# Kernel optimization log

Measured on AMD Instinct MI355X. Metric: run time of the kernel, lower is better.

Reference implementation:

```python
import jax, jax.numpy as jnp
import numpy as np

B, C_IN, C_OUT, H, W = 32, 256, 256, 56, 56
RATE = 0.5
K = int(C_OUT * (1.0 - RATE))  # 128 channels zeroed
BN_EPS = 1e-5


def setup_inputs() -> dict:
    key = jax.random.key(0)
    ks = jax.random.split(key, 4)
    return {
        "x": jax.random.normal(ks[0], (B, C_IN, H, W), dtype=jnp.float32),
        "conv_w": jax.random.normal(ks[1], (C_OUT, C_IN, 3, 3), dtype=jnp.float32) * 0.05,
        "gate_w": jax.random.normal(ks[2], (C_OUT, C_IN), dtype=jnp.float32) * 0.05,
        "gate_b": jnp.ones((C_OUT,), dtype=jnp.float32),
        "bn_gamma": jnp.ones((C_OUT,), dtype=jnp.float32),
        "bn_beta": jnp.zeros((C_OUT,), dtype=jnp.float32),
        "bn_mean": jnp.zeros((C_OUT,), dtype=jnp.float32),
        "bn_var": jnp.ones((C_OUT,), dtype=jnp.float32),
    }


def reference(x, conv_w, gate_w, gate_b, bn_gamma, bn_beta, bn_mean, bn_var):
    # conv2: 3x3, stride 1, padding 1, no bias  -> [B, C_OUT, H, W]
    y = jax.lax.conv_general_dilated(
        x, conv_w, window_strides=(1, 1), padding=((1, 1), (1, 1)),
        dimension_numbers=("NCHW", "OIHW", "NCHW"))
    # BatchNorm2d (eval mode: running stats)
    inv = bn_gamma / jnp.sqrt(bn_var + BN_EPS)
    y = y * inv[None, :, None, None] + (bn_beta - bn_mean * inv)[None, :, None, None]
    # use_relu=True
    y = jax.nn.relu(y)
    # gate: global abs-avg-pool -> linear -> relu   [B, C_OUT]
    s = jnp.mean(jnp.abs(x), axis=(2, 3))  # [B, C_IN]
    g = jax.nn.relu(s @ gate_w.T + gate_b)
    # zero the K smallest gate values per row (topk of -g), then renormalize
    _, idx = jax.lax.top_k(-g, K)  # indices of K smallest
    t = g.at[jnp.arange(B)[:, None], idx].set(0.0)
    t = t / jnp.sum(t, axis=1, keepdims=True) * C_OUT
    # broadcast channel mask
    return y * t[:, :, None, None]
```

## Files before the change

kernel.cpp:

```cpp
#include <hip/hip_runtime.h>
#include <hip/hip_bf16.h>
#include <cstdint>

typedef unsigned short ushort_t;
typedef unsigned int uint_t;
typedef __bf16 bf16x8 __attribute__((ext_vector_type(8)));
typedef float f32x4 __attribute__((ext_vector_type(4)));

#define B_SZ 32
#define C_IN 256
#define C_OUT 256
#define H_SZ 56
#define W_SZ 56
#define HW 3136
#define HP 58
#define WP 58
#define BN_EPS 1e-5f
#define K_ZERO 128

__device__ __forceinline__ ushort_t f2bf(float f) {
    unsigned int u = __builtin_bit_cast(unsigned int, f);
    unsigned int r = (u + 0x7fffu + ((u >> 16) & 1u)) >> 16;
    return (ushort_t)r;
}

__device__ __forceinline__ void load_lds16(const void* gptr, void* ldsptr) {
    __builtin_amdgcn_global_load_lds(
        (const __attribute__((address_space(1))) unsigned int*)(uintptr_t)gptr,
        (__attribute__((address_space(3))) unsigned int*)(uintptr_t)ldsptr,
        16, 0, 0);
}

__global__ __launch_bounds__(256) void prep_x_kernel(const float* __restrict__ x,
                                                     ushort_t* __restrict__ xbp,
                                                     float* __restrict__ s) {
    const int cit = blockIdx.x, h = blockIdx.y, b = blockIdx.z;
    __shared__ float tile[64][57];
    __shared__ float red2[256];
    const int t = threadIdx.x;
    const float* src = x + ((size_t)(b * C_IN + cit * 64) * H_SZ + h) * W_SZ;
    for (int i = t; i < 64 * 14; i += 256) {
        int ci = i / 14, w4 = (i - ci * 14) * 4;
        float4 v = *(const float4*)(src + (size_t)ci * HW + w4);
        tile[ci][w4] = v.x; tile[ci][w4 + 1] = v.y;
        tile[ci][w4 + 2] = v.z; tile[ci][w4 + 3] = v.w;
    }
    __syncthreads();
    {
        int ci = t & 63, wg = t >> 6;
        float a = 0.f;
#pragma unroll
        for (int j = 0; j < 14; j++) a += fabsf(tile[ci][wg * 14 + j]);
        red2[t] = a;
    }
    __syncthreads();
    if (t < 64) {
        float tot = red2[t] + red2[t + 64] + red2[t + 128] + red2[t + 192];
        atomicAdd(&s[b * C_IN + cit * 64 + t], tot * (1.0f / (float)HW));
    }
    for (int i = t; i < W_SZ * 16; i += 256) {
        int w = i >> 4, c4 = (i & 15) * 4;
        uint_t lo = (uint_t)f2bf(tile[c4][w])     | ((uint_t)f2bf(tile[c4 + 1][w]) << 16);
        uint_t hi = (uint_t)f2bf(tile[c4 + 2][w]) | ((uint_t)f2bf(tile[c4 + 3][w]) << 16);
        size_t dst = ((size_t)((b * HP + h + 1) * WP + (w + 1))) * C_IN + cit * 64 + c4;
        *(uint2*)&xbp[dst] = make_uint2(lo, hi);
    }
}

__global__ __launch_bounds__(256) void prep_w_kernel(const float* __restrict__ w,
                                                     const float* __restrict__ gamma,
                                                     const float* __restrict__ beta,
                                                     const float* __restrict__ mean,
                                                     const float* __restrict__ var,
                                                     ushort_t* __restrict__ Wt,
                                                     float* __restrict__ bninv,
                                                     float* __restrict__ bnadd) {
    int idx = blockIdx.x * 256 + threadIdx.x;
    if (idx < 9 * C_OUT * C_IN) {
        int tap = idx >> 16;
        int rem = idx & 65535;
        int co = rem >> 8, ci = rem & 255;
        Wt[idx] = f2bf(w[(size_t)(co * C_IN + ci) * 9 + tap]);
    }
    if (blockIdx.x == 0 && threadIdx.x < C_OUT) {
        int c = threadIdx.x;
        float inv = gamma[c] * rsqrtf(var[c] + BN_EPS);
        bninv[c] = inv;
        bnadd[c] = beta[c] - mean[c] * inv;
    }
}

__global__ __launch_bounds__(256) void gate_kernel(const float* __restrict__ s,
                                                   const float* __restrict__ gw,
                                                   const float* __restrict__ gb,
                                                   float* __restrict__ tscale) {
    const int b = blockIdx.x, t = threadIdx.x;
    __shared__ float sh_s[C_IN], sh_g[C_OUT], red[256];
    sh_s[t] = s[b * C_IN + t];
    __syncthreads();
    float acc = gb[t];
    const float* wr = gw + (size_t)t * C_IN;
    for (int ci = 0; ci < C_IN; ci++) acc += sh_s[ci] * wr[ci];
    float g = fmaxf(acc, 0.f);
    sh_g[t] = g;
    __syncthreads();
    int cnt = 0;
    for (int j = 0; j < C_OUT; j++) {
        float gj = sh_g[j];
        cnt += (gj < g) || (gj == g && j < t);
    }
    float tv = (cnt >= K_ZERO) ? g : 0.f;
    red[t] = tv;
    __syncthreads();
    for (int off = 128; off > 0; off >>= 1) {
        if (t < off) red[t] += red[t + off];
        __syncthreads();
    }
    tscale[b * C_OUT + t] = tv * ((float)C_OUT / red[0]);
}

__global__ __launch_bounds__(256) void conv_kernel(const ushort_t* __restrict__ xbp,
                                                   const ushort_t* __restrict__ Wt,
                                                   const float* __restrict__ bninv,
                                                   const float* __restrict__ bnadd,
                                                   const float* __restrict__ tscale,
                                                   float* __restrict__ out) {
    __shared__ __align__(16) ushort_t As[128 * 64];
    __shared__ __align__(16) ushort_t Bs[128 * 64];
    const int t = threadIdx.x;
    const int bx = blockIdx.x;
    const int by = blockIdx.y;
    const int lane = t & 63;
    const int wv = t >> 6;
    const int waveM = wv >> 1, waveN = wv & 1;

    const int srow = t >> 3;
    const int gxor8 = ((t & 7) ^ (srow & 7)) * 8;
    int arow[4], wrow[4];
#pragma unroll
    for (int i = 0; i < 4; i++) {
        int p = bx * 128 + i * 32 + srow;
        int b = p / HW;
        int r = p - b * HW;
        int hh = r / W_SZ, ww = r - hh * W_SZ;
        arow[i] = ((b * HP + hh + 1) * WP + (ww + 1)) * C_IN + gxor8;
        wrow[i] = (by * 128 + i * 32 + srow) * C_IN + gxor8;
    }
    ushort_t* ldsA = As + t * 8;
    ushort_t* ldsB = Bs + t * 8;

    int aoff[2][4], boff[2][4];
#pragma unroll
    for (int ks = 0; ks < 2; ks++)
#pragma unroll
        for (int mt = 0; mt < 4; mt++) {
            int c = (lane >> 4) + ks * 4;
            int ra = waveM * 64 + mt * 16 + (lane & 15);
            aoff[ks][mt] = (ra * 8 + (c ^ (ra & 7))) * 16;
            int rb = waveN * 64 + mt * 16 + (lane & 15);
            boff[ks][mt] = (rb * 8 + (c ^ (rb & 7))) * 16;
        }

    f32x4 acc[4][4];
#pragma unroll
    for (int i = 0; i < 4; i++)
#pragma unroll
        for (int j = 0; j < 4; j++) acc[i][j] = (f32x4){0.f, 0.f, 0.f, 0.f};

    const char* Ab = (const char*)As;
    const char* Bb = (const char*)Bs;

    for (int tap = 0; tap < 9; tap++) {
        const int doff = ((tap / 3 - 1) * WP + (tap % 3 - 1)) * C_IN;
        const int woff = tap * (C_OUT * C_IN);
#pragma unroll
        for (int cq = 0; cq < 4; cq++) {
            const int ci0 = cq * 64;
#pragma unroll
            for (int i = 0; i < 4; i++) {
                load_lds16(xbp + arow[i] + doff + ci0, ldsA + i * 2048);
                load_lds16(Wt + wrow[i] + woff + ci0, ldsB + i * 2048);
            }
            __syncthreads();
#pragma unroll
            for (int ks = 0; ks < 2; ks++) {
                bf16x8 af[4], bf[4];
#pragma unroll
                for (int mt = 0; mt < 4; mt++) af[mt] = *(const bf16x8*)(Ab + aoff[ks][mt]);
#pragma unroll
                for (int nt = 0; nt < 4; nt++) bf[nt] = *(const bf16x8*)(Bb + boff[ks][nt]);
#pragma unroll
                for (int mt = 0; mt < 4; mt++)
#pragma unroll
                    for (int nt = 0; nt < 4; nt++)
                        acc[mt][nt] = __builtin_amdgcn_mfma_f32_16x16x32_bf16(
                            af[mt], bf[nt], acc[mt][nt], 0, 0, 0);
            }
            __syncthreads();
        }
    }

#pragma unroll
    for (int mt = 0; mt < 4; mt++) {
        int p0 = bx * 128 + waveM * 64 + mt * 16 + (lane >> 4) * 4;
        int b = p0 / HW;
        int hw = p0 - b * HW;
#pragma unroll
        for (int nt = 0; nt < 4; nt++) {
            int co = by * 128 + waveN * 64 + nt * 16 + (lane & 15);
            float inv = bninv[co], add = bnadd[co], tsc = tscale[b * C_OUT + co];
            float4 o;
            o.x = fmaxf(acc[mt][nt][0] * inv + add, 0.f) * tsc;
            o.y = fmaxf(acc[mt][nt][1] * inv + add, 0.f) * tsc;
            o.z = fmaxf(acc[mt][nt][2] * inv + add, 0.f) * tsc;
            o.w = fmaxf(acc[mt][nt][3] * inv + add, 0.f) * tsc;
            *(float4*)(out + (size_t)(b * C_OUT + co) * HW + hw) = o;
        }
    }
}

extern "C" void kernel_launch(void* const* d_in, const int* in_sizes, int n_in,
                              void* d_out, int out_size, void* d_ws, size_t ws_size,
                              hipStream_t stream) {
    const float* x      = (const float*)d_in[0];
    const float* conv_w = (const float*)d_in[1];
    const float* gate_w = (const float*)d_in[2];
    const float* gate_b = (const float*)d_in[3];
    const float* bn_g   = (const float*)d_in[4];
    const float* bn_b   = (const float*)d_in[5];
    const float* bn_m   = (const float*)d_in[6];
    const float* bn_v   = (const float*)d_in[7];
    float* out = (float*)d_out;

    char* ws = (char*)d_ws;
    float*    s      = (float*)(ws + 0);
    float*    tscale = (float*)(ws + 32768);
    float*    bninv  = (float*)(ws + 65536);
    float*    bnadd  = (float*)(ws + 66560);
    ushort_t* Wt     = (ushort_t*)(ws + 67584);
    ushort_t* xbp    = (ushort_t*)(ws + 1247232);

    hipMemsetAsync(s, 0, 32768, stream);
    hipMemsetAsync(xbp, 0, (size_t)B_SZ * HP * WP * C_IN * 2, stream);
    prep_x_kernel<<<dim3(4, 56, 32), 256, 0, stream>>>(x, xbp, s);
    prep_w_kernel<<<2304, 256, 0, stream>>>(conv_w, bn_g, bn_b, bn_m, bn_v, Wt, bninv, bnadd);
    gate_kernel<<<32, 256, 0, stream>>>(s, gate_w, gate_b, tscale);
    conv_kernel<<<dim3(784, 2), 256, 0, stream>>>(xbp, Wt, bninv, bnadd, tscale, out);
}
```

Before: 385.2 us.

## Drop workspace memsets, zero halo in-kernel, swizzle conv grid, add occupancy hint

Removes the two hipMemsetAsync calls. The gate-sum buffer is now zeroed inside prep_w, which runs first, and prep_x writes zeros only to the padded halo border of the bf16 input instead of clearing the whole padded tensor. The conv grid becomes a flat 1D launch whose block index is remapped so that pairs of output-channel tiles sharing the same pixel tile run next to each other, which should improve L2 reuse. launch_bounds also gains a minimum of 3 blocks per CU, which may force register spilling.

```diff
diff --git a/kernel.cpp b/kernel.cpp
--- a/kernel.cpp
+++ b/kernel.cpp
@@ -29,6 +29,31 @@
         (const __attribute__((address_space(1))) unsigned int*)(uintptr_t)gptr,
         (__attribute__((address_space(3))) unsigned int*)(uintptr_t)ldsptr,
         16, 0, 0);
+}
+
+__global__ __launch_bounds__(256) void prep_w_kernel(const float* __restrict__ w,
+                                                     const float* __restrict__ gamma,
+                                                     const float* __restrict__ beta,
+                                                     const float* __restrict__ mean,
+                                                     const float* __restrict__ var,
+                                                     ushort_t* __restrict__ Wt,
+                                                     float* __restrict__ bninv,
+                                                     float* __restrict__ bnadd,
+                                                     float* __restrict__ s) {
+    int idx = blockIdx.x * 256 + threadIdx.x;
+    if (idx < 9 * C_OUT * C_IN) {
+        int tap = idx >> 16;
+        int rem = idx & 65535;
+        int co = rem >> 8, ci = rem & 255;
+        Wt[idx] = f2bf(w[(size_t)(co * C_IN + ci) * 9 + tap]);
+    }
+    if (blockIdx.x < 32) s[idx] = 0.f;
+    if (blockIdx.x == 32 && threadIdx.x < C_OUT) {
+        int c = threadIdx.x;
+        float inv = gamma[c] * rsqrtf(var[c] + BN_EPS);
+        bninv[c] = inv;
+        bnadd[c] = beta[c] - mean[c] * inv;
+    }
 }
 
 __global__ __launch_bounds__(256) void prep_x_kernel(const float* __restrict__ x,
@@ -58,6 +83,7 @@
         float tot = red2[t] + red2[t + 64] + red2[t + 128] + red2[t + 192];
         atomicAdd(&s[b * C_IN + cit * 64 + t], tot * (1.0f / (float)HW));
     }
+    const uint2 z2 = make_uint2(0u, 0u);
     for (int i = t; i < W_SZ * 16; i += 256) {
         int w = i >> 4, c4 = (i & 15) * 4;
         uint_t lo = (uint_t)f2bf(tile[c4][w])     | ((uint_t)f2bf(tile[c4 + 1][w]) << 16);
@@ -65,28 +91,18 @@
         size_t dst = ((size_t)((b * HP + h + 1) * WP + (w + 1))) * C_IN + cit * 64 + c4;
         *(uint2*)&xbp[dst] = make_uint2(lo, hi);
     }
-}
-
-__global__ __launch_bounds__(256) void prep_w_kernel(const float* __restrict__ w,
-                                                     const float* __restrict__ gamma,
-                                                     const float* __restrict__ beta,
-                                                     const float* __restrict__ mean,
-                                                     const float* __restrict__ var,
-                                                     ushort_t* __restrict__ Wt,
-                                                     float* __restrict__ bninv,
-                                                     float* __restrict__ bnadd) {
-    int idx = blockIdx.x * 256 + threadIdx.x;
-    if (idx < 9 * C_OUT * C_IN) {
-        int tap = idx >> 16;
-        int rem = idx & 65535;
-        int co = rem >> 8, ci = rem & 255;
-        Wt[idx] = f2bf(w[(size_t)(co * C_IN + ci) * 9 + tap]);
-    }
-    if (blockIdx.x == 0 && threadIdx.x < C_OUT) {
-        int c = threadIdx.x;
-        float inv = gamma[c] * rsqrtf(var[c] + BN_EPS);
-        bninv[c] = inv;
-        bnadd[c] = beta[c] - mean[c] * inv;
+    if (t < 32) {
+        int side = t >> 4, c4 = (t & 15) * 4;
+        size_t dst = ((size_t)((b * HP + h + 1) * WP + side * 57)) * C_IN + cit * 64 + c4;
+        *(uint2*)&xbp[dst] = z2;
+    }
+    if (h == 0 || h == 55) {
+        int prow = (h == 0) ? 0 : 57;
+        for (int i = t; i < 58 * 16; i += 256) {
+            int w = i >> 4, c4 = (i & 15) * 4;
+            size_t dst = ((size_t)((b * HP + prow) * WP + w)) * C_IN + cit * 64 + c4;
+            *(uint2*)&xbp[dst] = z2;
+        }
     }
 }
 
@@ -119,17 +135,18 @@
     tscale[b * C_OUT + t] = tv * ((float)C_OUT / red[0]);
 }
 
-__global__ __launch_bounds__(256) void conv_kernel(const ushort_t* __restrict__ xbp,
-                                                   const ushort_t* __restrict__ Wt,
-                                                   const float* __restrict__ bninv,
-                                                   const float* __restrict__ bnadd,
-                                                   const float* __restrict__ tscale,
-                                                   float* __restrict__ out) {
+__global__ __launch_bounds__(256, 3) void conv_kernel(const ushort_t* __restrict__ xbp,
+                                                      const ushort_t* __restrict__ Wt,
+                                                      const float* __restrict__ bninv,
+                                                      const float* __restrict__ bnadd,
+                                                      const float* __restrict__ tscale,
+                                                      float* __restrict__ out) {
     __shared__ __align__(16) ushort_t As[128 * 64];
     __shared__ __align__(16) ushort_t Bs[128 * 64];
     const int t = threadIdx.x;
-    const int bx = blockIdx.x;
-    const int by = blockIdx.y;
+    const int bxr = blockIdx.x;
+    const int bx = (bxr >> 4) * 8 + (bxr & 7);
+    const int by = (bxr >> 3) & 1;
     const int lane = t & 63;
     const int wv = t >> 6;
     const int waveM = wv >> 1, waveN = wv & 1;
@@ -151,15 +168,16 @@
 
     int aoff[2][4], boff[2][4];
 #pragma unroll
-    for (int ks = 0; ks < 2; ks++)
+    for (int ks = 0; ks < 2; ks++) {
+        int c = (lane >> 4) + ks * 4;
 #pragma unroll
         for (int mt = 0; mt < 4; mt++) {
-            int c = (lane >> 4) + ks * 4;
             int ra = waveM * 64 + mt * 16 + (lane & 15);
             aoff[ks][mt] = (ra * 8 + (c ^ (ra & 7))) * 16;
             int rb = waveN * 64 + mt * 16 + (lane & 15);
             boff[ks][mt] = (rb * 8 + (c ^ (rb & 7))) * 16;
         }
+    }
 
     f32x4 acc[4][4];
 #pragma unroll
@@ -240,10 +258,8 @@
     ushort_t* Wt     = (ushort_t*)(ws + 67584);
     ushort_t* xbp    = (ushort_t*)(ws + 1247232);
 
-    hipMemsetAsync(s, 0, 32768, stream);
-    hipMemsetAsync(xbp, 0, (size_t)B_SZ * HP * WP * C_IN * 2, stream);
+    prep_w_kernel<<<2304, 256, 0, stream>>>(conv_w, bn_g, bn_b, bn_m, bn_v, Wt, bninv, bnadd, s);
     prep_x_kernel<<<dim3(4, 56, 32), 256, 0, stream>>>(x, xbp, s);
-    prep_w_kernel<<<2304, 256, 0, stream>>>(conv_w, bn_g, bn_b, bn_m, bn_v, Wt, bninv, bnadd);
     gate_kernel<<<32, 256, 0, stream>>>(s, gate_w, gate_b, tscale);
-    conv_kernel<<<dim3(784, 2), 256, 0, stream>>>(xbp, Wt, bninv, bnadd, tscale, out);
-}
+    conv_kernel<<<1568, 256, 0, stream>>>(xbp, Wt, bninv, bnadd, tscale, out);
+}
```

After: 350.4 us. -9.0%, faster.
